# Performance work log

Measured on AMD Instinct MI355X. Metric: run time of the kernel, lower is better.

The kernel has to match this reference:

```python
import jax, jax.numpy as jnp
import numpy as np


def _hard_sigmoid(x):
    # Keras ConvLSTM2D default recurrent_activation
    return jnp.clip(0.2 * x + 0.5, 0.0, 1.0)


def _conv(x, w):
    # NHWC input, HWIO kernel, SAME padding, stride 1
    return jax.lax.conv_general_dilated(
        x, w, (1, 1), 'SAME', dimension_numbers=('NHWC', 'HWIO', 'NHWC'))


def _convlstm(seq, h, c, k, rk, b):
    # seq: [B, T, H, W, Cin]; h, c: [B, H, W, F]
    # k: [kh, kw, Cin, 4F], rk: [kh, kw, F, 4F], b: [4F]
    def step(carry, x):
        h, c = carry
        z = _conv(x, k) + _conv(h, rk) + b  # [B,H,W,4F]
        zi, zf, zc, zo = jnp.split(z, 4, axis=-1)
        i = _hard_sigmoid(zi)
        f = _hard_sigmoid(zf)
        o = _hard_sigmoid(zo)
        c = f * c + i * jnp.tanh(zc)
        h = o * jnp.tanh(c)
        return (h, c), None
    (h, c), _ = jax.lax.scan(step, (h, c), jnp.swapaxes(seq, 0, 1))
    return h, c


def setup_inputs() -> dict:
    key = jax.random.key(0)
    ks = jax.random.split(key, 14)
    B, T, H, W, Cin, F, K = 32, 1, 64, 64, 1, 64, 3
    s = 0.05
    inp = {
        'input_': jax.random.normal(ks[0], (B, T, H, W, Cin), jnp.float32),
        'h0': jax.random.normal(ks[1], (B, H, W, F), jnp.float32) * s,
        'c0': jax.random.normal(ks[2], (B, H, W, F), jnp.float32) * s,
        'h1': jax.random.normal(ks[3], (B, H, W, F), jnp.float32) * s,
        'c1': jax.random.normal(ks[4], (B, H, W, F), jnp.float32) * s,
        'k0': jax.random.normal(ks[5], (K, K, Cin, 4 * F), jnp.float32) * s,
        'rk0': jax.random.normal(ks[6], (K, K, F, 4 * F), jnp.float32) * s,
        'b0': jnp.zeros((4 * F,), jnp.float32),
        'k1': jax.random.normal(ks[7], (K, K, F, 4 * F), jnp.float32) * s,
        'rk1': jax.random.normal(ks[8], (K, K, F, 4 * F), jnp.float32) * s,
        'b1': jnp.zeros((4 * F,), jnp.float32),
        'cw': jax.random.normal(ks[9], (1, 1, F, 1), jnp.float32) * s,
        'cb': jnp.zeros((1,), jnp.float32),
    }
    return inp


def reference(input_, h0, c0, h1, c1, k0, rk0, b0, k1, rk1, b1, cw, cb):
    # Layer 0 consumes the input frame sequence (T=1)
    h0n, c0n = _convlstm(input_, h0, c0, k0, rk0, b0)
    # Layer 1 consumes layer-0's last hidden state as its (length-1) input
    h1n, c1n = _convlstm(h0n[:, None], h1, c1, k1, rk1, b1)
    frames = _conv(h1n, cw) + cb  # 1x1 conv head -> [B,H,W,1]
    return frames, h0n, c0n, h1n, c1n
```

## Files before the change

### kernel.cpp

```cpp
#include <hip/hip_runtime.h>
#include <hip/hip_bf16.h>

typedef short s16;
typedef __attribute__((ext_vector_type(8))) short bf16x8;
typedef __attribute__((ext_vector_type(4))) float f32x4;

__device__ __forceinline__ s16 f2bf(float f) {
  unsigned u = __builtin_bit_cast(unsigned, f);
  unsigned r = (u + 0x7FFFu + ((u >> 16) & 1u)) >> 16;
  return (s16)r;
}

__device__ __forceinline__ float hsig(float x) {
  return fminf(fmaxf(0.2f * x + 0.5f, 0.0f), 1.0f);
}

__global__ void wprep_kernel(const float* __restrict__ rk0, const float* __restrict__ k1,
                             const float* __restrict__ rk1, const float* __restrict__ k0,
                             s16* __restrict__ w0t, s16* __restrict__ w1t,
                             s16* __restrict__ w2t, s16* __restrict__ k0t) {
  int idx = blockIdx.x * 256 + threadIdx.x;
  const int n1 = 9 * 256 * 64;
  if (idx < 3 * n1) {
    int which = idx / n1;
    int r = idx - which * n1;
    int ic = r & 63;
    int oc = (r >> 6) & 255;
    int tap = r >> 14;
    const float* src = (which == 0) ? rk0 : (which == 1) ? k1 : rk1;
    s16* dst = (which == 0) ? w0t : (which == 1) ? w1t : w2t;
    dst[r] = f2bf(src[(tap * 64 + ic) * 256 + oc]);
  } else if (idx < 3 * n1 + 8192) {
    int r = idx - 3 * n1;
    int kk = r & 31;
    int oc = r >> 5;
    k0t[r] = (kk < 9) ? f2bf(k0[kk * 256 + oc]) : (s16)0;
  }
}

#define PXS 66
#define ROWSZ (PXS * 64)
#define SRCSZ (6 * ROWSZ)
template <bool F32>
__device__ __forceinline__ bf16x8 load_conv8(const void* src, long off) {
  if constexpr (F32) {
    const float* p = (const float*)src + off;
    float4 v0 = *reinterpret_cast<const float4*>(p);
    float4 v1 = *reinterpret_cast<const float4*>(p + 4);
    bf16x8 r;
    r[0] = f2bf(v0.x); r[1] = f2bf(v0.y); r[2] = f2bf(v0.z); r[3] = f2bf(v0.w);
    r[4] = f2bf(v1.x); r[5] = f2bf(v1.y); r[6] = f2bf(v1.z); r[7] = f2bf(v1.w);
    return r;
  } else {
    return *reinterpret_cast<const bf16x8*>((const s16*)src + off);
  }
}

template <int NSRC, bool XPATH, bool S0F32, bool S1F32>
__global__ __launch_bounds__(1024, 4) void cell_kernel(
    const void* __restrict__ src0,
    const void* __restrict__ src1,
    const s16* __restrict__ w0,
    const s16* __restrict__ w1,
    const float* __restrict__ xin,
    const s16* __restrict__ k0t,
    const float* __restrict__ bias,
    const float* __restrict__ c_old,
    float* __restrict__ h_out,
    float* __restrict__ c_out,
    s16* __restrict__ hb_out)
{
  __shared__ __align__(16) s16 a_lds[NSRC * SRCSZ];
  __shared__ __align__(16) s16 w_lds[3][8192];
  __shared__ float x_lds[XPATH ? 384 : 1];

  const int tid = threadIdx.x;
  const int b  = blockIdx.x >> 4;
  const int y0 = (blockIdx.x & 15) << 2;

  #pragma unroll
  for (int i = 0; i < 3; ++i) {
    int c   = tid + i * 1024;
    int row = c >> 9;
    int px  = (c >> 3) & 63;
    int cb  = c & 7;
    int y   = y0 - 1 + row;
    int xp  = px + 1;
    long goff = ((long)(b * 64 + y) * 64 + px) * 64 + cb * 8;
    int  doff = (row * PXS + xp) * 64 + ((cb ^ (xp & 7)) * 8);
    bf16x8 v0 = {};
    if ((unsigned)y < 64u) v0 = load_conv8<S0F32>(src0, goff);
    *reinterpret_cast<bf16x8*>(a_lds + doff) = v0;
    if (NSRC == 2) {
      bf16x8 v1 = {};
      if ((unsigned)y < 64u) v1 = load_conv8<S1F32>(src1, goff);
      *reinterpret_cast<bf16x8*>(a_lds + SRCSZ + doff) = v1;
    }
  }
  if (tid < NSRC * 96) {
    int s   = tid / 96;
    int r   = tid % 96;
    int row = r >> 4;
    int xp  = ((r >> 3) & 1) ? 65 : 0;
    int cb  = r & 7;
    bf16x8 z = {};
    *reinterpret_cast<bf16x8*>(a_lds + s * SRCSZ + (row * PXS + xp) * 64 + cb * 8) = z;
  }
  if (XPATH) {
    if (tid < 384) {
      int row = tid >> 6, px = tid & 63;
      int y = y0 - 1 + row;
      x_lds[tid] = ((unsigned)y < 64u) ? xin[(b * 64 + y) * 64 + px] : 0.0f;
    }
  }

  const int wave = tid >> 6;
  const int lane = tid & 63;
  const int g    = wave & 3;
  const int mh   = wave >> 2;
  const int l15  = lane & 15;
  const int l4   = lane >> 4;

  constexpr int NST = NSRC * 18;
  const int w_goff = (tid & 255) * 64 + (tid >> 8) * 8;
  char* wl0 = (char*)(&w_lds[0][0]) + ((tid >> 6) << 10);
  auto issueW = [&](int u) {
    int uu = (u >= NST) ? u - NST : u;
    int t2 = uu >> 1, k = uu & 1;
    int si  = (NSRC == 2 && t2 >= 9) ? 1 : 0;
    int tap = t2 - 9 * si;
    const s16* wt = (si ? w1 : w0) + tap * 16384 + k * 32 + w_goff;
    char* dst = wl0 + (uu % 3) * 16384;
    __builtin_amdgcn_global_load_lds((const __attribute__((address_space(1))) void*)wt,
                                     (__attribute__((address_space(3))) void*)dst, 16, 0, 0);
  };

  issueW(0);
  issueW(1);
  __syncthreads();

  f32x4 acc[4][4] = {};

  if (XPATH) {
    bf16x8 bx[4];
    #pragma unroll
    for (int j = 0; j < 4; ++j) {
      int oc = j * 64 + g * 16 + l15;
      bx[j] = *reinterpret_cast<const bf16x8*>(k0t + oc * 32 + l4 * 8);
    }
    #pragma unroll
    for (int m = 0; m < 4; ++m) {
      int px = m * 16 + l15;
      bf16x8 ax = {};
      #pragma unroll
      for (int j = 0; j < 8; ++j) {
        int t = l4 * 8 + j;
        if (t < 9) {
          int dy = t / 3, dx = t - dy * 3;
          int xx = px + dx - 1;
          float xv = ((unsigned)xx < 64u) ? x_lds[(mh + dy) * 64 + xx] : 0.0f;
          ax[j] = f2bf(xv);
        }
      }
      #pragma unroll
      for (int j = 0; j < 4; ++j)
        acc[m][j] = __builtin_amdgcn_mfma_f32_16x16x32_bf16(ax, bx[j], acc[m][j], 0, 0, 0);
    }
  }

  const char* wbuf  = (const char*)(&w_lds[0][0]);
  const int   wroff = l4 * 4096;
  auto readW = [&](bf16x8* wf, int slot) {
    const char* wb = wbuf + slot * 16384 + wroff;
    #pragma unroll
    for (int j = 0; j < 4; ++j) {
      int oc = j * 64 + g * 16 + l15;
      wf[j] = *reinterpret_cast<const bf16x8*>(wb + oc * 16);
    }
  };
  auto doStage = [&](const bf16x8* wf, int u) {
    int t2 = u >> 1, k = u & 1;
    int si  = (NSRC == 2 && t2 >= 9) ? 1 : 0;
    int tap = t2 - 9 * si;
    int dy = tap / 3, dx = tap - dy * 3;
    const char* lb = (const char*)a_lds + si * (SRCSZ * 2) + (mh + dy) * (ROWSZ * 2);
    #pragma unroll
    for (int m = 0; m < 4; ++m) {
      int xq   = m * 16 + l15 + dx;
      int boff = xq * 128 + (((k << 6) | (l4 << 4)) ^ ((xq & 7) << 4));
      bf16x8 a = *reinterpret_cast<const bf16x8*>(lb + boff);
      #pragma unroll
      for (int j = 0; j < 4; ++j)
        acc[m][j] = __builtin_amdgcn_mfma_f32_16x16x32_bf16(a, wf[j], acc[m][j], 0, 0, 0);
    }
  };

  bf16x8 wfA[4], wfB[4];
  readW(wfA, 0);
  #pragma unroll
  for (int u = 0; u < NST; u += 2) {
    issueW(u + 2);
    readW(wfB, (u + 1) % 3);
    doStage(wfA, u);
    asm volatile("s_waitcnt vmcnt(0)" ::: "memory");
    __builtin_amdgcn_s_barrier();
    issueW(u + 3);
    readW(wfA, (u + 2) % 3);
    doStage(wfB, u + 1);
    asm volatile("s_waitcnt vmcnt(0)" ::: "memory");
    __builtin_amdgcn_s_barrier();
  }

  float bi[4];
  #pragma unroll
  for (int j = 0; j < 4; ++j) bi[j] = bias[j * 64 + g * 16 + l15];

  const int pix_base = b * 4096 + y0 * 64;
  const int f = g * 16 + l15;
  #pragma unroll
  for (int m = 0; m < 4; ++m) {
    #pragma unroll
    for (int r = 0; r < 4; ++r) {
      int pl = mh * 64 + m * 16 + l4 * 4 + r;
      int off = (pix_base + pl) * 64 + f;
      float zi = acc[m][0][r] + bi[0];
      float zf = acc[m][1][r] + bi[1];
      float zc = acc[m][2][r] + bi[2];
      float zo = acc[m][3][r] + bi[3];
      float ig = hsig(zi), fg = hsig(zf), og = hsig(zo);
      float cn = fg * c_old[off] + ig * tanhf(zc);
      float hn = og * tanhf(cn);
      c_out[off] = cn;
      h_out[off] = hn;
      if (hb_out) hb_out[off] = f2bf(hn);
    }
  }
}

__global__ void frames_kernel(const float* __restrict__ h, const float* __restrict__ cw,
                              const float* __restrict__ cbp, float* __restrict__ out) {
  int tid = blockIdx.x * 256 + threadIdx.x;
  int p  = tid >> 2;
  int fc = (tid & 3) * 16;
  const float4* hp = reinterpret_cast<const float4*>(h + p * 64 + fc);
  const float4* wp = reinterpret_cast<const float4*>(cw + fc);
  float s = 0.0f;
  #pragma unroll
  for (int i = 0; i < 4; ++i) {
    float4 v = hp[i];
    float4 w = wp[i];
    s += v.x * w.x + v.y * w.y + v.z * w.z + v.w * w.w;
  }
  s += __shfl_xor(s, 1);
  s += __shfl_xor(s, 2);
  if ((tid & 3) == 0) out[p] = s + cbp[0];
}

extern "C" void kernel_launch(void* const* d_in, const int* in_sizes, int n_in,
                              void* d_out, int out_size, void* d_ws, size_t ws_size,
                              hipStream_t stream) {
  const float* x   = (const float*)d_in[0];
  const float* h0  = (const float*)d_in[1];
  const float* c0  = (const float*)d_in[2];
  const float* h1  = (const float*)d_in[3];
  const float* c1  = (const float*)d_in[4];
  const float* k0  = (const float*)d_in[5];
  const float* rk0 = (const float*)d_in[6];
  const float* b0  = (const float*)d_in[7];
  const float* k1  = (const float*)d_in[8];
  const float* rk1 = (const float*)d_in[9];
  const float* b1  = (const float*)d_in[10];
  const float* cw  = (const float*)d_in[11];
  const float* cbp = (const float*)d_in[12];

  float* out    = (float*)d_out;
  float* frames = out;
  float* h0n    = out + 131072;
  float* c0n    = out + 131072 + 8388608;
  float* h1n    = out + 131072 + 2 * 8388608;
  float* c1n    = out + 131072 + 3 * 8388608;

  char* ws = (char*)d_ws;
  const size_t SZ_H = 16777216;
  s16* h0nb = (s16*)(ws + 0 * SZ_H);
  s16* w0t  = (s16*)(ws + 1 * SZ_H);
  s16* w1t  = (s16*)(ws + 1 * SZ_H + 1 * 294912);
  s16* w2t  = (s16*)(ws + 1 * SZ_H + 2 * 294912);
  s16* k0t  = (s16*)(ws + 1 * SZ_H + 3 * 294912);

  wprep_kernel<<<1760, 256, 0, stream>>>(rk0, k1, rk1, k0, w0t, w1t, w2t, k0t);

  cell_kernel<1, true, true, false><<<512, 1024, 0, stream>>>(
      h0, nullptr, w0t, nullptr, x, k0t, b0, c0, h0n, c0n, h0nb);

  cell_kernel<2, false, false, true><<<512, 1024, 0, stream>>>(
      h0nb, h1, w1t, w2t, nullptr, nullptr, b1, c1, h1n, c1n, nullptr);

  frames_kernel<<<2048, 256, 0, stream>>>(h1n, cw, cbp, frames);
}
```

Measured before the change: 209.0 us.

## Shrink cell tiles to 2 rows, 512 threads, double-buffered weights, sequential source staging

Each cell block now covers 2 output rows with 512 threads instead of 4 rows with 1024, doubling the grid to 1024 blocks. The weight ring buffer shrinks from triple to double buffering, with a barrier at the top of each stage and s_setprio around the MFMA section. For the two-source layer, the second source is staged into the same LDS buffer after the first 18 stages. This cuts LDS use per block so more blocks can stay resident. In exchange, each block reloads halo rows and the full weight set for half as much output, and the second source load is exposed instead of overlapped.

Result: slower. 344.8 us (+65.0%).

```diff
diff --git a/kernel.cpp b/kernel.cpp
--- a/kernel.cpp
+++ b/kernel.cpp
@@ -40,7 +40,8 @@
 
 #define PXS 66
 #define ROWSZ (PXS * 64)
-#define SRCSZ (6 * ROWSZ)
+#define ASZ (4 * ROWSZ)
+
 template <bool F32>
 __device__ __forceinline__ bf16x8 load_conv8(const void* src, long off) {
   if constexpr (F32) {
@@ -56,8 +57,32 @@
   }
 }
 
+template <bool F32>
+__device__ __forceinline__ void stage_src(s16* a_lds, const void* src, int b, int y0, int tid) {
+  #pragma unroll
+  for (int i = 0; i < 4; ++i) {
+    int c   = tid + i * 512;
+    int row = c >> 9;
+    int px  = (c >> 3) & 63;
+    int cb  = c & 7;
+    int y   = y0 - 1 + row;
+    int xp  = px + 1;
+    bf16x8 v = {};
+    if ((unsigned)y < 64u)
+      v = load_conv8<F32>(src, ((long)(b * 64 + y) * 64 + px) * 64 + cb * 8);
+    *reinterpret_cast<bf16x8*>(a_lds + (row * PXS + xp) * 64 + ((cb ^ (xp & 7)) * 8)) = v;
+  }
+  if (tid < 64) {
+    int row = tid >> 4;
+    int xp  = ((tid >> 3) & 1) ? 65 : 0;
+    int cb  = tid & 7;
+    bf16x8 z = {};
+    *reinterpret_cast<bf16x8*>(a_lds + (row * PXS + xp) * 64 + cb * 8) = z;
+  }
+}
+
 template <int NSRC, bool XPATH, bool S0F32, bool S1F32>
-__global__ __launch_bounds__(1024, 4) void cell_kernel(
+__global__ __launch_bounds__(512, 4) void cell_kernel(
     const void* __restrict__ src0,
     const void* __restrict__ src1,
     const s16* __restrict__ w0,
@@ -70,49 +95,13 @@
     float* __restrict__ c_out,
     s16* __restrict__ hb_out)
 {
-  __shared__ __align__(16) s16 a_lds[NSRC * SRCSZ];
-  __shared__ __align__(16) s16 w_lds[3][8192];
-  __shared__ float x_lds[XPATH ? 384 : 1];
+  __shared__ __align__(16) s16 a_lds[ASZ];
+  __shared__ __align__(16) s16 w_lds[2][8192];
+  __shared__ float x_lds[XPATH ? 256 : 1];
 
   const int tid = threadIdx.x;
-  const int b  = blockIdx.x >> 4;
-  const int y0 = (blockIdx.x & 15) << 2;
-
-  #pragma unroll
-  for (int i = 0; i < 3; ++i) {
-    int c   = tid + i * 1024;
-    int row = c >> 9;
-    int px  = (c >> 3) & 63;
-    int cb  = c & 7;
-    int y   = y0 - 1 + row;
-    int xp  = px + 1;
-    long goff = ((long)(b * 64 + y) * 64 + px) * 64 + cb * 8;
-    int  doff = (row * PXS + xp) * 64 + ((cb ^ (xp & 7)) * 8);
-    bf16x8 v0 = {};
-    if ((unsigned)y < 64u) v0 = load_conv8<S0F32>(src0, goff);
-    *reinterpret_cast<bf16x8*>(a_lds + doff) = v0;
-    if (NSRC == 2) {
-      bf16x8 v1 = {};
-      if ((unsigned)y < 64u) v1 = load_conv8<S1F32>(src1, goff);
-      *reinterpret_cast<bf16x8*>(a_lds + SRCSZ + doff) = v1;
-    }
-  }
-  if (tid < NSRC * 96) {
-    int s   = tid / 96;
-    int r   = tid % 96;
-    int row = r >> 4;
-    int xp  = ((r >> 3) & 1) ? 65 : 0;
-    int cb  = r & 7;
-    bf16x8 z = {};
-    *reinterpret_cast<bf16x8*>(a_lds + s * SRCSZ + (row * PXS + xp) * 64 + cb * 8) = z;
-  }
-  if (XPATH) {
-    if (tid < 384) {
-      int row = tid >> 6, px = tid & 63;
-      int y = y0 - 1 + row;
-      x_lds[tid] = ((unsigned)y < 64u) ? xin[(b * 64 + y) * 64 + px] : 0.0f;
-    }
-  }
+  const int b  = blockIdx.x >> 5;
+  const int y0 = (blockIdx.x & 31) << 1;
 
   const int wave = tid >> 6;
   const int lane = tid & 63;
@@ -122,24 +111,66 @@
   const int l4   = lane >> 4;
 
   constexpr int NST = NSRC * 18;
-  const int w_goff = (tid & 255) * 64 + (tid >> 8) * 8;
-  char* wl0 = (char*)(&w_lds[0][0]) + ((tid >> 6) << 10);
+
   auto issueW = [&](int u) {
-    int uu = (u >= NST) ? u - NST : u;
-    int t2 = uu >> 1, k = uu & 1;
+    int t2 = u >> 1, k = u & 1;
     int si  = (NSRC == 2 && t2 >= 9) ? 1 : 0;
     int tap = t2 - 9 * si;
-    const s16* wt = (si ? w1 : w0) + tap * 16384 + k * 32 + w_goff;
-    char* dst = wl0 + (uu % 3) * 16384;
-    __builtin_amdgcn_global_load_lds((const __attribute__((address_space(1))) void*)wt,
-                                     (__attribute__((address_space(3))) void*)dst, 16, 0, 0);
+    const s16* wt = (si ? w1 : w0) + tap * 16384 + k * 32;
+    char* wl = (char*)(&w_lds[u & 1][0]);
+    __builtin_amdgcn_global_load_lds(
+        (const __attribute__((address_space(1))) void*)(wt + (tid & 255) * 64 + (tid >> 8) * 8),
+        (__attribute__((address_space(3))) void*)(wl + (tid >> 6) * 1024), 16, 0, 0);
+    __builtin_amdgcn_global_load_lds(
+        (const __attribute__((address_space(1))) void*)(wt + (tid & 255) * 64 + ((tid >> 8) + 2) * 8),
+        (__attribute__((address_space(3))) void*)(wl + 8192 + (tid >> 6) * 1024), 16, 0, 0);
   };
 
+  auto readW = [&](bf16x8 (&wf)[4], int slot) {
+    const char* wb = (const char*)(&w_lds[slot][0]) + l4 * 4096;
+    #pragma unroll
+    for (int j = 0; j < 4; ++j) {
+      int oc = j * 64 + g * 16 + l15;
+      wf[j] = *reinterpret_cast<const bf16x8*>(wb + oc * 16);
+    }
+  };
+
+  f32x4 acc[4][4] = {};
+  bf16x8 wfA[4], wfB[4];
+
+  auto body = [&](bf16x8 (&wfC)[4], bf16x8 (&wfN)[4], int u) {
+    asm volatile("s_waitcnt vmcnt(0)" ::: "memory");
+    __builtin_amdgcn_s_barrier();
+    if (u + 2 < NST) issueW(u + 2);
+    if (u + 1 < NST) readW(wfN, (u + 1) & 1);
+    int t2 = u >> 1, k = u & 1;
+    int tap = (t2 >= 9) ? t2 - 9 : t2;
+    int dy = tap / 3, dx = tap - dy * 3;
+    const char* lb = (const char*)a_lds + (mh + dy) * (ROWSZ * 2);
+    __builtin_amdgcn_s_setprio(1);
+    #pragma unroll
+    for (int m = 0; m < 4; ++m) {
+      int xq   = m * 16 + l15 + dx;
+      int boff = xq * 128 + (((k << 6) | (l4 << 4)) ^ ((xq & 7) << 4));
+      bf16x8 a = *reinterpret_cast<const bf16x8*>(lb + boff);
+      #pragma unroll
+      for (int j = 0; j < 4; ++j)
+        acc[m][j] = __builtin_amdgcn_mfma_f32_16x16x32_bf16(a, wfC[j], acc[m][j], 0, 0, 0);
+    }
+    __builtin_amdgcn_s_setprio(0);
+  };
+
+  stage_src<S0F32>(a_lds, src0, b, y0, tid);
+  if (XPATH) {
+    if (tid < 256) {
+      int row = tid >> 6, px = tid & 63;
+      int y = y0 - 1 + row;
+      x_lds[tid] = ((unsigned)y < 64u) ? xin[(b * 64 + y) * 64 + px] : 0.0f;
+    }
+  }
   issueW(0);
   issueW(1);
   __syncthreads();
-
-  f32x4 acc[4][4] = {};
 
   if (XPATH) {
     bf16x8 bx[4];
@@ -156,9 +187,9 @@
       for (int j = 0; j < 8; ++j) {
         int t = l4 * 8 + j;
         if (t < 9) {
-          int dy = t / 3, dx = t - dy * 3;
-          int xx = px + dx - 1;
-          float xv = ((unsigned)xx < 64u) ? x_lds[(mh + dy) * 64 + xx] : 0.0f;
+          int dyt = t / 3, dxt = t - dyt * 3;
+          int xx = px + dxt - 1;
+          float xv = ((unsigned)xx < 64u) ? x_lds[(mh + dyt) * 64 + xx] : 0.0f;
           ax[j] = f2bf(xv);
         }
       }
@@ -168,47 +199,23 @@
     }
   }
 
-  const char* wbuf  = (const char*)(&w_lds[0][0]);
-  const int   wroff = l4 * 4096;
-  auto readW = [&](bf16x8* wf, int slot) {
-    const char* wb = wbuf + slot * 16384 + wroff;
-    #pragma unroll
-    for (int j = 0; j < 4; ++j) {
-      int oc = j * 64 + g * 16 + l15;
-      wf[j] = *reinterpret_cast<const bf16x8*>(wb + oc * 16);
-    }
-  };
-  auto doStage = [&](const bf16x8* wf, int u) {
-    int t2 = u >> 1, k = u & 1;
-    int si  = (NSRC == 2 && t2 >= 9) ? 1 : 0;
-    int tap = t2 - 9 * si;
-    int dy = tap / 3, dx = tap - dy * 3;
-    const char* lb = (const char*)a_lds + si * (SRCSZ * 2) + (mh + dy) * (ROWSZ * 2);
-    #pragma unroll
-    for (int m = 0; m < 4; ++m) {
-      int xq   = m * 16 + l15 + dx;
-      int boff = xq * 128 + (((k << 6) | (l4 << 4)) ^ ((xq & 7) << 4));
-      bf16x8 a = *reinterpret_cast<const bf16x8*>(lb + boff);
-      #pragma unroll
-      for (int j = 0; j < 4; ++j)
-        acc[m][j] = __builtin_amdgcn_mfma_f32_16x16x32_bf16(a, wf[j], acc[m][j], 0, 0, 0);
-    }
-  };
-
-  bf16x8 wfA[4], wfB[4];
   readW(wfA, 0);
-  #pragma unroll
-  for (int u = 0; u < NST; u += 2) {
-    issueW(u + 2);
-    readW(wfB, (u + 1) % 3);
-    doStage(wfA, u);
-    asm volatile("s_waitcnt vmcnt(0)" ::: "memory");
-    __builtin_amdgcn_s_barrier();
-    issueW(u + 3);
-    readW(wfA, (u + 2) % 3);
-    doStage(wfB, u + 1);
-    asm volatile("s_waitcnt vmcnt(0)" ::: "memory");
-    __builtin_amdgcn_s_barrier();
+
+  #pragma unroll
+  for (int i = 0; i < 18; ++i) {
+    if ((i & 1) == 0) body(wfA, wfB, i);
+    else              body(wfB, wfA, i);
+  }
+
+  if (NSRC == 2) {
+    __syncthreads();
+    stage_src<S1F32>(a_lds, src1, b, y0, tid);
+    __syncthreads();
+    #pragma unroll
+    for (int i = 18; i < 36; ++i) {
+      if ((i & 1) == 0) body(wfA, wfB, i);
+      else              body(wfB, wfA, i);
+    }
   }
 
   float bi[4];
@@ -290,10 +297,10 @@
 
   wprep_kernel<<<1760, 256, 0, stream>>>(rk0, k1, rk1, k0, w0t, w1t, w2t, k0t);
 
-  cell_kernel<1, true, true, false><<<512, 1024, 0, stream>>>(
+  cell_kernel<1, true, true, false><<<1024, 512, 0, stream>>>(
       h0, nullptr, w0t, nullptr, x, k0t, b0, c0, h0n, c0n, h0nb);
 
-  cell_kernel<2, false, false, true><<<512, 1024, 0, stream>>>(
+  cell_kernel<2, false, false, true><<<1024, 512, 0, stream>>>(
       h0nb, h1, w1t, w2t, nullptr, nullptr, b1, c1, h1n, c1n, nullptr);
 
   frames_kernel<<<2048, 256, 0, stream>>>(h1n, cw, cbp, frames);
```
